# Performance work log

Measured on AMD Instinct MI355X. Metric: run time of the kernel, lower is better.

Reference implementation:

```python
import jax, jax.numpy as jnp
import numpy as np

EPS = 1e-12  # matches F.normalize default eps
TEMPERATURE = 1.0  # normlized=False -> temperature reset to 1.0
W1, W3 = 1.0, 0.3
LAMBDA1, LAMBDA2 = 1.0, 1.0


def setup_inputs() -> dict:
    key = jax.random.key(0)
    kq, kp = jax.random.split(key)
    q_hidden = jax.random.normal(kq, (16, 64, 768), dtype=jnp.float32)
    p_hidden = jax.random.normal(kp, (128, 256, 768), dtype=jnp.float32)
    return {"q_hidden": q_hidden, "p_hidden": p_hidden}


def _l2norm(x):
    n = jnp.linalg.norm(x, axis=-1, keepdims=True)
    return x / jnp.maximum(n, EPS)


def _ce(scores, target):
    # nn.CrossEntropyLoss(reduction='mean')
    ls = jax.nn.log_softmax(scores, axis=-1)
    return -jnp.mean(ls[jnp.arange(scores.shape[0]), target])


def _kld_log_target_batchmean(inp_log, tgt_log):
    # nn.KLDivLoss(reduction='batchmean', log_target=True)
    return jnp.sum(jnp.exp(tgt_log) * (tgt_log - inp_log)) / inp_log.shape[0]


def reference(q_hidden, p_hidden):
    # cls pooling (normlized=False -> no normalize of pooled reps)
    q_reps = q_hidden[:, 0]  # [Bq, D]
    p_reps = p_hidden[:, 0]  # [Bp, D]

    # multivector maxsim over normalized token embeddings
    qn = _l2norm(q_hidden)  # [Bq, Lq, D]
    pn = _l2norm(p_hidden)  # [Bp, Lp, D]
    sim = jnp.einsum('qid,pjd->qpij', qn, pn)  # [Bq, Bp, Lq, Lp]
    mv_scores = jnp.max(jnp.max(sim, axis=-1), axis=-1)  # [Bq, Bp]

    # in-batch-negative contrastive path (training)
    scores = jnp.matmul(q_reps, p_reps.T) / TEMPERATURE  # [Bq, Bp]
    mv_scores = mv_scores / TEMPERATURE
    Bq = scores.shape[0]
    group_size = p_reps.shape[0] // Bq
    target = jnp.arange(Bq) * group_size

    s_inter = W1 * scores + W3 * mv_scores
    loss_dense1 = _ce(scores, target)
    loss_mulvec1 = _ce(mv_scores, target)
    loss_inter = _ce(s_inter, target)

    s_logits1 = jax.nn.log_softmax(scores, axis=1)
    s_logits2 = jax.nn.log_softmax(mv_scores, axis=1)
    t_logits = jax.nn.log_softmax(s_inter, axis=1)
    loss_dense2 = _kld_log_target_batchmean(s_logits1, t_logits)
    # NOTE: source overwrites loss_mulvec1 with the KLD term (faithful bug reproduction)
    loss_mulvec1 = _kld_log_target_batchmean(s_logits2, t_logits)

    L1 = 0.3 * (loss_dense1 * LAMBDA1 + loss_mulvec1 * LAMBDA2 + loss_inter)
    L2 = 0.2 * (loss_dense2 * LAMBDA1 + loss_mulvec1 * LAMBDA2)
    loss = (L1 + L2) * 0.5
    return loss
```

## Files before the change

kernel.cpp:

```cpp
#include <hip/hip_runtime.h>
#include <hip/hip_bf16.h>

#define D   768
#define NQ  16
#define NP  128
#define QI  64
#define PJ  256
#define MQ  (NQ*QI)
#define MP  (NP*PJ)

typedef __attribute__((ext_vector_type(8)))  int   int8v;
typedef __attribute__((ext_vector_type(16))) float floatx16;

#define LDS_AS __attribute__((address_space(3)))
#define GLB_AS __attribute__((address_space(1)))

static __device__ __forceinline__ void async_copy16(const uchar* g, uchar* l) {
    __builtin_amdgcn_global_load_lds((const GLB_AS uint32_t*)g,
                                     (LDS_AS uint32_t*)l, 16, 0, 0);
}

static __device__ __forceinline__ uint pack_fp8(float a, float b, float c, float d) {
    uint r = __builtin_amdgcn_cvt_pk_fp8_f32(a, b, 0, false);
    r      = __builtin_amdgcn_cvt_pk_fp8_f32(c, d, r, true);
    return r;
}

__global__ __launch_bounds__(256) void norm_rows(const float* __restrict__ ph,
                                                 const float* __restrict__ qh,
                                                 uchar* __restrict__ P8,
                                                 uchar* __restrict__ Q8) {
    int row = blockIdx.x * 4 + (threadIdx.x >> 6);
    const float* in; uchar* out;
    if (row < MP) { in = ph; out = P8; }
    else          { in = qh; out = Q8; row -= MP; }
    const int lane = threadIdx.x & 63;
    const float4* r4 = (const float4*)(in + (size_t)row * D);

    float4 x0 = r4[lane], x1 = r4[lane + 64], x2 = r4[lane + 128];
    float ss = x0.x*x0.x + x0.y*x0.y + x0.z*x0.z + x0.w*x0.w
             + x1.x*x1.x + x1.y*x1.y + x1.z*x1.z + x1.w*x1.w
             + x2.x*x2.x + x2.y*x2.y + x2.z*x2.z + x2.w*x2.w;
    #pragma unroll
    for (int o = 32; o > 0; o >>= 1) ss += __shfl_xor(ss, o, 64);
    float inv = 1.0f / fmaxf(sqrtf(ss), 1e-12f);

    uint* o4 = (uint*)(out + (size_t)row * D);
    o4[lane]       = pack_fp8(x0.x*inv, x0.y*inv, x0.z*inv, x0.w*inv);
    o4[lane + 64]  = pack_fp8(x1.x*inv, x1.y*inv, x1.z*inv, x1.w*inv);
    o4[lane + 128] = pack_fp8(x2.x*inv, x2.y*inv, x2.z*inv, x2.w*inv);
}

#define SCALE1 0x7F7F7F7Fu

static __device__ __forceinline__ int8v ld_frag(const uchar* base, int off0, int off1) {
    uint4 u0 = *(const uint4*)(base + off0);
    uint4 u1 = *(const uint4*)(base + off1);
    int8v v;
    v[0] = u0.x; v[1] = u0.y; v[2] = u0.z; v[3] = u0.w;
    v[4] = u1.x; v[5] = u1.y; v[6] = u1.z; v[7] = u1.w;
    return v;
}

__global__ __launch_bounds__(256, 2) void sim_max_kernel(const uchar* __restrict__ Q8,
                                                         const uchar* __restrict__ P8,
                                                         float* __restrict__ mv) {
    const int p  = blockIdx.x;
    const int qp = blockIdx.y;
    __shared__ uchar lA[128 * 128];
    __shared__ uchar lB[256 * 128];
    __shared__ float smax[4];

    const int t = threadIdx.x;
    const int wave = t >> 6, lane = t & 63;
    const int qi = wave >> 1, pj = wave & 1;

    const int lrow = lane >> 3;
    const int dmaoff = lrow * D + (((lane & 7) ^ lrow) << 4);

    const int r  = lane & 31;
    const int kh = lane >> 5;
    const int rx = r & 7;

    const uchar* Abase = Q8 + (size_t)(qp * 128) * D;
    const uchar* Bbase = P8 + (size_t)p * PJ * D;

    floatx16 acc[2][4];
    #pragma unroll
    for (int i = 0; i < 2; i++)
        #pragma unroll
        for (int j = 0; j < 4; j++)
            #pragma unroll
            for (int e = 0; e < 16; e++) acc[i][j][e] = 0.f;

    for (int k0 = 0; k0 < D; k0 += 128) {
        __syncthreads();
        #pragma unroll
        for (int g = 0; g < 4; g++) {
            const int R0 = wave * 32 + g * 8;
            async_copy16(Abase + (size_t)R0 * D + k0 + dmaoff, lA + R0 * 128);
        }
        #pragma unroll
        for (int g = 0; g < 8; g++) {
            const int R0 = wave * 64 + g * 8;
            async_copy16(Bbase + (size_t)R0 * D + k0 + dmaoff, lB + R0 * 128);
        }
        __syncthreads();

        #pragma unroll
        for (int s = 0; s < 2; s++) {
            const int c0 = s * 4 + kh * 2;
            const int o0 = ((c0     ^ rx) << 4);
            const int o1 = (((c0|1) ^ rx) << 4);
            int8v a[2];
            #pragma unroll
            for (int i = 0; i < 2; i++) {
                const uchar* rp = lA + (qi * 64 + i * 32 + r) * 128;
                a[i] = ld_frag(rp, o0, o1);
            }
            #pragma unroll
            for (int j = 0; j < 4; j++) {
                const uchar* rp = lB + (pj * 128 + j * 32 + r) * 128;
                int8v b = ld_frag(rp, o0, o1);
                #pragma unroll
                for (int i = 0; i < 2; i++)
                    acc[i][j] = __builtin_amdgcn_mfma_scale_f32_32x32x64_f8f6f4(
                        a[i], b, acc[i][j], 0, 0, 0, SCALE1, 0, SCALE1);
            }
        }
    }

    float m = -1e30f;
    #pragma unroll
    for (int i = 0; i < 2; i++)
        #pragma unroll
        for (int j = 0; j < 4; j++)
            #pragma unroll
            for (int e = 0; e < 16; e++) m = fmaxf(m, acc[i][j][e]);
    #pragma unroll
    for (int o = 32; o > 0; o >>= 1) m = fmaxf(m, __shfl_xor(m, o, 64));
    if (lane == 0) smax[wave] = m;
    __syncthreads();
    if (t < 2)
        mv[(qp * 2 + t) * NP + p] = fmaxf(smax[2 * t], smax[2 * t + 1]);
}

__global__ __launch_bounds__(256) void scores_kernel(const float* __restrict__ qh,
                                                     const float* __restrict__ ph,
                                                     float* __restrict__ scores) {
    const int wave = threadIdx.x >> 6, lane = threadIdx.x & 63;
    const int bid = blockIdx.x * 4 + wave;
    const int q = bid >> 7, p = bid & 127;
    const float4* qr = (const float4*)(qh + (size_t)q * QI * D);
    const float4* pr = (const float4*)(ph + (size_t)p * PJ * D);
    float s = 0.f;
    #pragma unroll
    for (int k = 0; k < 3; k++) {
        float4 a = qr[lane + k * 64], b = pr[lane + k * 64];
        s += a.x * b.x + a.y * b.y + a.z * b.z + a.w * b.w;
    }
    #pragma unroll
    for (int o = 32; o > 0; o >>= 1) s += __shfl_xor(s, o, 64);
    if (lane == 0) scores[q * NP + p] = s;
}

__global__ __launch_bounds__(64) void loss_kernel(const float* __restrict__ scores,
                                                  const float* __restrict__ mv,
                                                  float* __restrict__ out) {
    const int lane = threadIdx.x;
    float ce_s = 0.f, ce_t = 0.f, kld_s = 0.f, kld_m = 0.f;

    for (int q = 0; q < NQ; q++) {
        const float* srow = scores + q * NP;
        const float* mrow = mv + q * NP;
        float s0 = srow[lane], s1 = srow[lane + 64];
        float m0 = mrow[lane], m1 = mrow[lane + 64];
        float t0 = s0 + 0.3f * m0, t1 = s1 + 0.3f * m1;

        float xs = fmaxf(s0, s1), xm = fmaxf(m0, m1), xt = fmaxf(t0, t1);
        #pragma unroll
        for (int o = 32; o > 0; o >>= 1) {
            xs = fmaxf(xs, __shfl_xor(xs, o, 64));
            xm = fmaxf(xm, __shfl_xor(xm, o, 64));
            xt = fmaxf(xt, __shfl_xor(xt, o, 64));
        }
        float es = expf(s0 - xs) + expf(s1 - xs);
        float em = expf(m0 - xm) + expf(m1 - xm);
        float et = expf(t0 - xt) + expf(t1 - xt);
        #pragma unroll
        for (int o = 32; o > 0; o >>= 1) {
            es += __shfl_xor(es, o, 64);
            em += __shfl_xor(em, o, 64);
            et += __shfl_xor(et, o, 64);
        }
        float lse_s = xs + logf(es), lse_m = xm + logf(em), lse_t = xt + logf(et);

        float ls0 = s0 - lse_s, ls1 = s1 - lse_s;
        float lm0 = m0 - lse_m, lm1 = m1 - lse_m;
        float lt0 = t0 - lse_t, lt1 = t1 - lse_t;
        float pt0 = expf(lt0), pt1 = expf(lt1);
        kld_s += pt0 * (lt0 - ls0) + pt1 * (lt1 - ls1);
        kld_m += pt0 * (lt0 - lm0) + pt1 * (lt1 - lm1);

        const int tgt = q * (NP / NQ);
        if (lane == (tgt & 63)) {
            if (tgt < 64) { ce_s -= ls0; ce_t -= lt0; }
            else          { ce_s -= ls1; ce_t -= lt1; }
        }
    }
    #pragma unroll
    for (int o = 32; o > 0; o >>= 1) {
        ce_s  += __shfl_xor(ce_s, o, 64);
        ce_t  += __shfl_xor(ce_t, o, 64);
        kld_s += __shfl_xor(kld_s, o, 64);
        kld_m += __shfl_xor(kld_m, o, 64);
    }
    if (lane == 0) {
        ce_s /= 16.f; ce_t /= 16.f; kld_s /= 16.f; kld_m /= 16.f;
        float L1 = 0.3f * (ce_s + kld_m + ce_t);
        float L2 = 0.2f * (kld_s + kld_m);
        out[0] = 0.5f * (L1 + L2);
    }
}

extern "C" void kernel_launch(void* const* d_in, const int* in_sizes, int n_in,
                              void* d_out, int out_size, void* d_ws, size_t ws_size,
                              hipStream_t stream) {
    const float* qh = (const float*)d_in[0];
    const float* ph = (const float*)d_in[1];

    char* ws = (char*)d_ws;
    uchar* P8 = (uchar*)ws;
    uchar* Q8 = (uchar*)(ws + (size_t)MP * D);
    float* mv = (float*)(ws + (size_t)MP * D + (size_t)MQ * D);
    float* scores = mv + NQ * NP;

    norm_rows<<<(MP + MQ) / 4, 256, 0, stream>>>(ph, qh, P8, Q8);
    sim_max_kernel<<<dim3(NP, 8), 256, 0, stream>>>(Q8, P8, mv);
    scores_kernel<<<512, 256, 0, stream>>>(qh, ph, scores);
    loss_kernel<<<1, 64, 0, stream>>>(scores, mv, (float*)d_out);
}
```

Measured before the change: 196.0 us.

## Quantize normalized embeddings to FP4 and fuse scores into norm kernel

Normalized token embeddings are now encoded as 4-bit e2m1 values with a hand-written rounding encoder. The maxsim GEMM runs MFMA in FP4 mode with a block scale, which halves the quantized buffer size, the global-to-LDS traffic and the K-loop iterations. The dense CLS score computation is merged into the normalization launch as extra blocks, removing one kernel launch. FP4 loses a lot of precision in the similarity maxima, so the loss may drift from the reference tolerance. The fp4 fragments are also only half-filled, with the upper four registers zeroed.

```diff
diff --git a/kernel.cpp b/kernel.cpp
--- a/kernel.cpp
+++ b/kernel.cpp
@@ -2,12 +2,14 @@
 #include <hip/hip_bf16.h>
 
 #define D   768
+#define D2  384
 #define NQ  16
 #define NP  128
 #define QI  64
 #define PJ  256
 #define MQ  (NQ*QI)
 #define MP  (NP*PJ)
+#define NROWBLK ((MP + MQ) / 4)
 
 typedef __attribute__((ext_vector_type(8)))  int   int8v;
 typedef __attribute__((ext_vector_type(16))) float floatx16;
@@ -20,50 +22,76 @@
                                      (LDS_AS uint32_t*)l, 16, 0, 0);
 }
 
-static __device__ __forceinline__ uint pack_fp8(float a, float b, float c, float d) {
-    uint r = __builtin_amdgcn_cvt_pk_fp8_f32(a, b, 0, false);
-    r      = __builtin_amdgcn_cvt_pk_fp8_f32(c, d, r, true);
+static __device__ __forceinline__ uint enc4(float4 v, float inv) {
+    uint r = 0;
+    const float* f = (const float*)&v;
+    #pragma unroll
+    for (int i = 0; i < 4; i++) {
+        float x = f[i] * inv;
+        float y = fabsf(x) * 16.0f;
+        uint c;
+        if (y < 2.25f) c = (uint)(int)rintf(y + y);
+        else           c = y < 3.5f ? 5u : (y < 5.0f ? 6u : 7u);
+        c |= (__float_as_uint(x) >> 28) & 8u;
+        r |= c << (4 * i);
+    }
     return r;
 }
 
-__global__ __launch_bounds__(256) void norm_rows(const float* __restrict__ ph,
-                                                 const float* __restrict__ qh,
-                                                 uchar* __restrict__ P8,
-                                                 uchar* __restrict__ Q8) {
-    int row = blockIdx.x * 4 + (threadIdx.x >> 6);
-    const float* in; uchar* out;
-    if (row < MP) { in = ph; out = P8; }
-    else          { in = qh; out = Q8; row -= MP; }
-    const int lane = threadIdx.x & 63;
-    const float4* r4 = (const float4*)(in + (size_t)row * D);
-
-    float4 x0 = r4[lane], x1 = r4[lane + 64], x2 = r4[lane + 128];
-    float ss = x0.x*x0.x + x0.y*x0.y + x0.z*x0.z + x0.w*x0.w
-             + x1.x*x1.x + x1.y*x1.y + x1.z*x1.z + x1.w*x1.w
-             + x2.x*x2.x + x2.y*x2.y + x2.z*x2.z + x2.w*x2.w;
-    #pragma unroll
-    for (int o = 32; o > 0; o >>= 1) ss += __shfl_xor(ss, o, 64);
-    float inv = 1.0f / fmaxf(sqrtf(ss), 1e-12f);
-
-    uint* o4 = (uint*)(out + (size_t)row * D);
-    o4[lane]       = pack_fp8(x0.x*inv, x0.y*inv, x0.z*inv, x0.w*inv);
-    o4[lane + 64]  = pack_fp8(x1.x*inv, x1.y*inv, x1.z*inv, x1.w*inv);
-    o4[lane + 128] = pack_fp8(x2.x*inv, x2.y*inv, x2.z*inv, x2.w*inv);
-}
-
-#define SCALE1 0x7F7F7F7Fu
-
-static __device__ __forceinline__ int8v ld_frag(const uchar* base, int off0, int off1) {
-    uint4 u0 = *(const uint4*)(base + off0);
-    uint4 u1 = *(const uint4*)(base + off1);
+__global__ __launch_bounds__(256) void norm_scores(const float* __restrict__ ph,
+                                                   const float* __restrict__ qh,
+                                                   uchar* __restrict__ P4,
+                                                   uchar* __restrict__ Q4,
+                                                   float* __restrict__ scores) {
+    const int wave = threadIdx.x >> 6, lane = threadIdx.x & 63;
+    if (blockIdx.x < NROWBLK) {
+        int row = blockIdx.x * 4 + wave;
+        const float* in; uchar* out;
+        if (row < MP) { in = ph; out = P4; }
+        else          { in = qh; out = Q4; row -= MP; }
+        const float4* r4 = (const float4*)(in + (size_t)row * D);
+
+        float4 x0 = r4[lane], x1 = r4[lane + 64], x2 = r4[lane + 128];
+        float ss = x0.x*x0.x + x0.y*x0.y + x0.z*x0.z + x0.w*x0.w
+                 + x1.x*x1.x + x1.y*x1.y + x1.z*x1.z + x1.w*x1.w
+                 + x2.x*x2.x + x2.y*x2.y + x2.z*x2.z + x2.w*x2.w;
+        #pragma unroll
+        for (int o = 32; o > 0; o >>= 1) ss += __shfl_xor(ss, o, 64);
+        float inv = 1.0f / fmaxf(sqrtf(ss), 1e-12f);
+
+        ushort* o2 = (ushort*)(out + (size_t)row * D2);
+        o2[lane]       = (ushort)enc4(x0, inv);
+        o2[lane + 64]  = (ushort)enc4(x1, inv);
+        o2[lane + 128] = (ushort)enc4(x2, inv);
+    } else {
+        const int bid = (blockIdx.x - NROWBLK) * 4 + wave;
+        const int q = bid >> 7, p = bid & 127;
+        const float4* qr = (const float4*)(qh + (size_t)q * QI * D);
+        const float4* pr = (const float4*)(ph + (size_t)p * PJ * D);
+        float s = 0.f;
+        #pragma unroll
+        for (int k = 0; k < 3; k++) {
+            float4 a = qr[lane + k * 64], b = pr[lane + k * 64];
+            s += a.x * b.x + a.y * b.y + a.z * b.z + a.w * b.w;
+        }
+        #pragma unroll
+        for (int o = 32; o > 0; o >>= 1) s += __shfl_xor(s, o, 64);
+        if (lane == 0) scores[q * NP + p] = s;
+    }
+}
+
+#define SCALE16 0x7B7B7B7Bu
+
+static __device__ __forceinline__ int8v ld_frag4(const uchar* rowp, int off) {
+    uint4 u = *(const uint4*)(rowp + off);
     int8v v;
-    v[0] = u0.x; v[1] = u0.y; v[2] = u0.z; v[3] = u0.w;
-    v[4] = u1.x; v[5] = u1.y; v[6] = u1.z; v[7] = u1.w;
+    v[0] = u.x; v[1] = u.y; v[2] = u.z; v[3] = u.w;
+    v[4] = 0;   v[5] = 0;   v[6] = 0;   v[7] = 0;
     return v;
 }
 
-__global__ __launch_bounds__(256, 2) void sim_max_kernel(const uchar* __restrict__ Q8,
-                                                         const uchar* __restrict__ P8,
+__global__ __launch_bounds__(256, 2) void sim_max_kernel(const uchar* __restrict__ Q4,
+                                                         const uchar* __restrict__ P4,
                                                          float* __restrict__ mv) {
     const int p  = blockIdx.x;
     const int qp = blockIdx.y;
@@ -76,14 +104,14 @@
     const int qi = wave >> 1, pj = wave & 1;
 
     const int lrow = lane >> 3;
-    const int dmaoff = lrow * D + (((lane & 7) ^ lrow) << 4);
+    const int dmaoff = lrow * D2 + (((lane & 7) ^ lrow) << 4);
 
     const int r  = lane & 31;
     const int kh = lane >> 5;
     const int rx = r & 7;
 
-    const uchar* Abase = Q8 + (size_t)(qp * 128) * D;
-    const uchar* Bbase = P8 + (size_t)p * PJ * D;
+    const uchar* Abase = Q4 + (size_t)(qp * 128) * D2;
+    const uchar* Bbase = P4 + (size_t)p * PJ * D2;
 
     floatx16 acc[2][4];
     #pragma unroll
@@ -93,39 +121,34 @@
             #pragma unroll
             for (int e = 0; e < 16; e++) acc[i][j][e] = 0.f;
 
-    for (int k0 = 0; k0 < D; k0 += 128) {
+    for (int k0 = 0; k0 < D2; k0 += 128) {
         __syncthreads();
         #pragma unroll
         for (int g = 0; g < 4; g++) {
             const int R0 = wave * 32 + g * 8;
-            async_copy16(Abase + (size_t)R0 * D + k0 + dmaoff, lA + R0 * 128);
+            async_copy16(Abase + (size_t)R0 * D2 + k0 + dmaoff, lA + R0 * 128);
         }
         #pragma unroll
         for (int g = 0; g < 8; g++) {
             const int R0 = wave * 64 + g * 8;
-            async_copy16(Bbase + (size_t)R0 * D + k0 + dmaoff, lB + R0 * 128);
+            async_copy16(Bbase + (size_t)R0 * D2 + k0 + dmaoff, lB + R0 * 128);
         }
         __syncthreads();
 
         #pragma unroll
-        for (int s = 0; s < 2; s++) {
-            const int c0 = s * 4 + kh * 2;
-            const int o0 = ((c0     ^ rx) << 4);
-            const int o1 = (((c0|1) ^ rx) << 4);
+        for (int s = 0; s < 4; s++) {
+            const int off = ((s * 2 + kh) ^ rx) << 4;
             int8v a[2];
             #pragma unroll
-            for (int i = 0; i < 2; i++) {
-                const uchar* rp = lA + (qi * 64 + i * 32 + r) * 128;
-                a[i] = ld_frag(rp, o0, o1);
-            }
+            for (int i = 0; i < 2; i++)
+                a[i] = ld_frag4(lA + (qi * 64 + i * 32 + r) * 128, off);
             #pragma unroll
             for (int j = 0; j < 4; j++) {
-                const uchar* rp = lB + (pj * 128 + j * 32 + r) * 128;
-                int8v b = ld_frag(rp, o0, o1);
+                int8v b = ld_frag4(lB + (pj * 128 + j * 32 + r) * 128, off);
                 #pragma unroll
                 for (int i = 0; i < 2; i++)
                     acc[i][j] = __builtin_amdgcn_mfma_scale_f32_32x32x64_f8f6f4(
-                        a[i], b, acc[i][j], 0, 0, 0, SCALE1, 0, SCALE1);
+                        a[i], b, acc[i][j], 4, 4, 0, SCALE16, 0, SCALE16);
             }
         }
     }
@@ -143,25 +166,6 @@
     __syncthreads();
     if (t < 2)
         mv[(qp * 2 + t) * NP + p] = fmaxf(smax[2 * t], smax[2 * t + 1]);
-}
-
-__global__ __launch_bounds__(256) void scores_kernel(const float* __restrict__ qh,
-                                                     const float* __restrict__ ph,
-                                                     float* __restrict__ scores) {
-    const int wave = threadIdx.x >> 6, lane = threadIdx.x & 63;
-    const int bid = blockIdx.x * 4 + wave;
-    const int q = bid >> 7, p = bid & 127;
-    const float4* qr = (const float4*)(qh + (size_t)q * QI * D);
-    const float4* pr = (const float4*)(ph + (size_t)p * PJ * D);
-    float s = 0.f;
-    #pragma unroll
-    for (int k = 0; k < 3; k++) {
-        float4 a = qr[lane + k * 64], b = pr[lane + k * 64];
-        s += a.x * b.x + a.y * b.y + a.z * b.z + a.w * b.w;
-    }
-    #pragma unroll
-    for (int o = 32; o > 0; o >>= 1) s += __shfl_xor(s, o, 64);
-    if (lane == 0) scores[q * NP + p] = s;
 }
 
 __global__ __launch_bounds__(64) void loss_kernel(const float* __restrict__ scores,
@@ -230,13 +234,12 @@
     const float* ph = (const float*)d_in[1];
 
     char* ws = (char*)d_ws;
-    uchar* P8 = (uchar*)ws;
-    uchar* Q8 = (uchar*)(ws + (size_t)MP * D);
-    float* mv = (float*)(ws + (size_t)MP * D + (size_t)MQ * D);
+    uchar* P4 = (uchar*)ws;
+    uchar* Q4 = (uchar*)(ws + (size_t)MP * D2);
+    float* mv = (float*)(ws + (size_t)MP * D2 + (size_t)MQ * D2);
     float* scores = mv + NQ * NP;
 
-    norm_rows<<<(MP + MQ) / 4, 256, 0, stream>>>(ph, qh, P8, Q8);
-    sim_max_kernel<<<dim3(NP, 8), 256, 0, stream>>>(Q8, P8, mv);
-    scores_kernel<<<512, 256, 0, stream>>>(qh, ph, scores);
+    norm_scores<<<NROWBLK + 512, 256, 0, stream>>>(ph, qh, P4, Q4, scores);
+    sim_max_kernel<<<dim3(NP, 8), 256, 0, stream>>>(Q4, P4, mv);
     loss_kernel<<<1, 64, 0, stream>>>(scores, mv, (float*)d_out);
 }
```

Result: faster. 183.5 us (-6.4%).
